# Kernel tuning notes

Hardware: AMD Instinct MI355X
Metric: run time of the kernel (lower is better)

Reference implementation:

```python
import jax, jax.numpy as jnp
import numpy as np

TOP_K = 2
TEMPERATURE = 1.0


def setup_inputs() -> dict:
    key = jax.random.key(0)
    k1, k2, k3 = jax.random.split(key, 3)
    x = jax.random.normal(k1, (4, 2048, 2048), jnp.float32)
    # prototypes are top right-singular vectors of lora_A -> unit norm rows
    protos = jax.random.normal(k2, (8, 2048), jnp.float32)
    protos = protos / jnp.linalg.norm(protos, axis=-1, keepdims=True)
    # precomputed_W = stack of B @ A per expert, shape (E, out, in)
    W = jax.random.normal(k3, (8, 2048, 2048), jnp.float32) * 0.02
    return {"x": x, "prototypes": protos, "W": W, "scaling": 2}


def reference(x, prototypes, W, scaling):
    F_in = x.shape[-1]
    tok = x.reshape(-1, F_in)                      # (t, F)
    t = tok.shape[0]
    E = prototypes.shape[0]
    # Arrow routing: |<tok, proto_e>| similarity, keep top-k, softmax
    sim = jnp.abs(tok @ prototypes.T)              # (t, E)
    top_v, idx = jax.lax.top_k(sim, TOP_K)         # (t, k)
    neg_inf = jnp.asarray(-jnp.inf, tok.dtype)
    full_score = jnp.full((t, E), neg_inf, dtype=tok.dtype)
    full_score = full_score.at[jnp.arange(t)[:, None], idx].set(top_v)
    coeff = jax.nn.softmax(full_score / TEMPERATURE, axis=1)  # (t, E), zero off top-k
    # dense per-expert LoRA delta, then coefficient combine (as in source)
    W_tok = jnp.einsum('eoi,ti->eto', W, tok)      # (E, t, out)
    delta = jnp.einsum('te,eto->to', coeff, W_tok) # (t, out)
    delta = jnp.asarray(scaling, delta.dtype) * delta  # dropout = identity (eval)
    return delta.reshape(*x.shape[:-1], delta.shape[-1])
```

## Files before the change

kernel.cpp:

```cpp
#include <hip/hip_runtime.h>

#define T_TOK 8192
#define F_IN  2048
#define F_OUT 2048
#define N_EXP 8
#define NKS   (F_IN / 64)
#define MAXTILES 144
#define RT_TPB 16
#define ROUTE_BLOCKS (T_TOK / RT_TPB)
#define CVT_BLOCKS   2048

typedef __attribute__((ext_vector_type(8))) short    short8;
typedef __attribute__((ext_vector_type(4))) float    f32x4;
typedef __attribute__((ext_vector_type(8))) _Float16 half8;
typedef unsigned short ushort;

#define AS1 __attribute__((address_space(1)))
#define AS3 __attribute__((address_space(3)))
#define GLOAD16(g, l) __builtin_amdgcn_global_load_lds((const AS1 unsigned int*)(g), \
                                                       (AS3 unsigned int*)(l), 16, 0, 0)

__device__ inline ushort f2bf(float f) {
    unsigned u = __float_as_uint(f);
    u += 0x7FFFu + ((u >> 16) & 1u);
    return (ushort)(u >> 16);
}

__device__ inline void top2_store(const float* s, int ti, float sc,
                                  int* sh_ei, float (*sh_cf)[2]) {
    float v0 = -1.f; int i0 = 0;
    #pragma unroll
    for (int e = 0; e < N_EXP; ++e) {
        const float a = fabsf(s[e]);
        if (a > v0) { v0 = a; i0 = e; }
    }
    float v1 = -1.f; int i1 = 0;
    #pragma unroll
    for (int e = 0; e < N_EXP; ++e) {
        const float a = fabsf(s[e]);
        if (e != i0 && a > v1) { v1 = a; i1 = e; }
    }
    const float ex  = expf(v1 - v0);
    const float inv = 1.f / (1.f + ex);
    sh_ei[ti]    = i0 | (i1 << 16);
    sh_cf[ti][0] = sc * inv;
    sh_cf[ti][1] = sc * ex * inv;
}

__global__ __launch_bounds__(256) void route_cvt_kernel(
    const float* __restrict__ x, const float* __restrict__ protos,
    const int* __restrict__ scaling, ushort* __restrict__ xb,
    int* __restrict__ counts, int* __restrict__ lists, float* __restrict__ coeffs,
    int* __restrict__ pos, const float* __restrict__ W, ushort* __restrict__ Wb)
{
    __shared__ int   sh_ei[RT_TPB];
    __shared__ float sh_cf[RT_TPB][2];
    __shared__ int   sh_base[N_EXP];

    if (blockIdx.x >= ROUTE_BLOCKS) {
        const int n8 = N_EXP * F_OUT * F_IN / 8;
        for (int i = (blockIdx.x - ROUTE_BLOCKS) * 256 + threadIdx.x; i < n8;
             i += CVT_BLOCKS * 256) {
            const float4 a = ((const float4*)W)[i * 2 + 0];
            const float4 b = ((const float4*)W)[i * 2 + 1];
            uint4 v;
            v.x = f2bf(a.x) | ((unsigned)f2bf(a.y) << 16);
            v.y = f2bf(a.z) | ((unsigned)f2bf(a.w) << 16);
            v.z = f2bf(b.x) | ((unsigned)f2bf(b.y) << 16);
            v.w = f2bf(b.z) | ((unsigned)f2bf(b.w) << 16);
            ((uint4*)Wb)[i] = v;
        }
        return;
    }

    const int wave = threadIdx.x >> 6;
    const int lane = threadIdx.x & 63;
    const float sc = (float)(*scaling);

    for (int pr = 0; pr < 2; ++pr) {
        const int ti0  = wave * 4 + pr * 2;
        const int tok0 = blockIdx.x * RT_TPB + ti0;
        const float* xr0 = x  + (size_t)tok0 * F_IN;
        const float* xr1 = xr0 + F_IN;
        ushort*      xo0 = xb + (size_t)tok0 * F_IN;
        ushort*      xo1 = xo0 + F_IN;

        float s0[N_EXP] = {}, s1[N_EXP] = {};
        for (int c = 0; c < F_IN / 256; ++c) {
            const int off = c * 256 + lane * 4;
            const float4 a = *(const float4*)(xr0 + off);
            const float4 b = *(const float4*)(xr1 + off);
            uint2 ba, bb;
            ba.x = f2bf(a.x) | ((unsigned)f2bf(a.y) << 16);
            ba.y = f2bf(a.z) | ((unsigned)f2bf(a.w) << 16);
            bb.x = f2bf(b.x) | ((unsigned)f2bf(b.y) << 16);
            bb.y = f2bf(b.z) | ((unsigned)f2bf(b.w) << 16);
            *(uint2*)(xo0 + off) = ba;
            *(uint2*)(xo1 + off) = bb;
            #pragma unroll
            for (int e = 0; e < N_EXP; ++e) {
                const float4 pv = *(const float4*)(protos + e * F_IN + off);
                s0[e] += a.x * pv.x + a.y * pv.y + a.z * pv.z + a.w * pv.w;
                s1[e] += b.x * pv.x + b.y * pv.y + b.z * pv.z + b.w * pv.w;
            }
        }
        #pragma unroll
        for (int e = 0; e < N_EXP; ++e) {
            float v0 = s0[e], v1 = s1[e];
            #pragma unroll
            for (int off = 32; off; off >>= 1) {
                v0 += __shfl_down(v0, off, 64);
                v1 += __shfl_down(v1, off, 64);
            }
            s0[e] = v0; s1[e] = v1;
        }
        if (lane == 0) {
            top2_store(s0, ti0,     sc, sh_ei, sh_cf);
            top2_store(s1, ti0 + 1, sc, sh_ei, sh_cf);
        }
    }
    __syncthreads();

    if (threadIdx.x < 64) {
        const int  p      = threadIdx.x;
        const bool active = p < RT_TPB * 2;
        const int  ti = p >> 1, j = p & 1;
        const int  e  = active ? ((sh_ei[ti] >> (j * 16)) & 0xffff) : 0xff;
        int rank = 0;
        #pragma unroll
        for (int ee = 0; ee < N_EXP; ++ee) {
            const unsigned long long m = __ballot(active && (e == ee));
            if (e == ee)
                rank = __popcll(m & ((1ull << p) - 1ull));
            if (p == ee && m != 0ull)
                sh_base[ee] = atomicAdd(&counts[ee], (int)__popcll(m));
        }
        if (active) {
            const int position = sh_base[e] + rank;
            const int gidx  = e * T_TOK + position;
            const int token = blockIdx.x * RT_TPB + ti;
            lists [gidx] = token;
            coeffs[gidx] = sh_cf[ti][j];
            pos[token * 2 + j] = gidx;
        }
    }
}

__global__ void plan_kernel(const int* __restrict__ counts, int* __restrict__ pbase,
                            int* __restrict__ ntiles, int* __restrict__ desc) {
    if (threadIdx.x == 0) {
        int pb = 0, t = 0;
        for (int e = 0; e < N_EXP; ++e) {
            pbase[e] = pb;
            const int ne = counts[e];
            const int nt = (ne + 127) >> 7;
            for (int i = 0; i < nt; ++i) desc[t++] = (e << 8) | i;
            pb += ne;
        }
        *ntiles = t;
    }
}

__global__ __launch_bounds__(256, 2) void gemm_kernel(
    const ushort* __restrict__ xb, const ushort* __restrict__ Wb,
    const int* __restrict__ counts, const int* __restrict__ lists,
    const int* __restrict__ pbase, const int* __restrict__ ntiles,
    const int* __restrict__ desc, _Float16* __restrict__ delta)
{
    const int total = *ntiles * 8;
    const int chunk = (total + 7) >> 3;
    const int xcd   = blockIdx.x & 7;
    const int j     = blockIdx.x >> 3;
    const int w     = xcd * chunk + j;
    if (j >= chunk || w >= total) return;
    const int ti = w >> 3;
    const int oi = w & 7;

    const int d     = desc[ti];
    const int e     = d >> 8;
    const int tile  = d & 255;
    const int n_e   = counts[e];
    const int tbase = tile << 7;
    const int o0    = oi * 256;
    const int prow0 = pbase[e] + tbase;

    __shared__ __align__(16) ushort As[128 * 64];
    __shared__ __align__(16) ushort Bs[256 * 64];

    const int tid  = threadIdx.x;
    const int lane = tid & 63;
    const int wid  = tid >> 6;
    const int wr   = wid >> 1, wc = wid & 1;

    const int ksrc = ((lane & 7) ^ (lane >> 3)) * 8;
    const ushort* srcA[4];
    #pragma unroll
    for (int g = 0; g < 4; ++g) {
        const int row  = g * 32 + wid * 8 + (lane >> 3);
        const int slot = min(tbase + row, n_e - 1);
        srcA[g] = xb + (size_t)lists[e * T_TOK + slot] * F_IN + ksrc;
    }
    const ushort* srcB = Wb + ((size_t)(e * F_OUT + o0 + wid * 8 + (lane >> 3))) * F_IN + ksrc;

    const int octx8 = ((lane >> 4) ^ (lane & 7)) * 8;
    const int ai    = (wr * 64  + (lane & 15)) * 64 + octx8;
    const int bi    = (wc * 128 + (lane & 15)) * 64 + octx8;

    f32x4 acc[4][8] = {};

    for (int ks = 0; ks < NKS; ++ks) {
        __syncthreads();
        #pragma unroll
        for (int g = 0; g < 4; ++g) {
            GLOAD16(srcA[g], As + (g * 32 + wid * 8) * 64);
            srcA[g] += 64;
        }
        #pragma unroll
        for (int g = 0; g < 8; ++g)
            GLOAD16(srcB + (size_t)g * 32 * F_IN, Bs + (g * 32 + wid * 8) * 64);
        srcB += 64;
        __syncthreads();

        short8 a[4][2], b[8][2];
        #pragma unroll
        for (int m = 0; m < 4; ++m) {
            a[m][0] = *(const short8*)(As + (ai + m * 1024));
            a[m][1] = *(const short8*)(As + ((ai + m * 1024) ^ 32));
        }
        #pragma unroll
        for (int n = 0; n < 8; ++n) {
            b[n][0] = *(const short8*)(Bs + (bi + n * 1024));
            b[n][1] = *(const short8*)(Bs + ((bi + n * 1024) ^ 32));
        }
        #pragma unroll
        for (int kk = 0; kk < 2; ++kk)
            #pragma unroll
            for (int m = 0; m < 4; ++m)
                #pragma unroll
                for (int n = 0; n < 8; ++n)
                    acc[m][n] = __builtin_amdgcn_mfma_f32_16x16x32_bf16(
                        a[m][kk], b[n][kk], acc[m][n], 0, 0, 0);
    }

    const int rl = (lane >> 4) * 4;
    const int cl = lane & 15;
    #pragma unroll
    for (int m = 0; m < 4; ++m)
        #pragma unroll
        for (int rr = 0; rr < 4; ++rr) {
            const int srow = wr * 64 + m * 16 + rl + rr;
            if (tbase + srow < n_e) {
                _Float16* drow = delta + (size_t)(prow0 + srow) * F_OUT + o0 + wc * 128 + cl;
                #pragma unroll
                for (int n = 0; n < 8; ++n)
                    drow[n * 16] = (_Float16)acc[m][n][rr];
            }
        }
}

__global__ __launch_bounds__(256) void combine_kernel(
    const _Float16* __restrict__ delta, const int* __restrict__ pos,
    const float* __restrict__ coeffs, const int* __restrict__ pbase,
    float* __restrict__ out)
{
    const int tok = blockIdx.x;
    const int id0 = pos[tok * 2 + 0];
    const int id1 = pos[tok * 2 + 1];
    const float cf0 = coeffs[id0];
    const float cf1 = coeffs[id1];
    const int r0 = pbase[id0 >> 13] + (id0 & (T_TOK - 1));
    const int r1 = pbase[id1 >> 13] + (id1 & (T_TOK - 1));
    const int c  = threadIdx.x * 8;

    const half8 a = *(const half8*)(delta + (size_t)r0 * F_OUT + c);
    const half8 b = *(const half8*)(delta + (size_t)r1 * F_OUT + c);
    float4 o0, o1;
    o0.x = cf0 * (float)a[0] + cf1 * (float)b[0];
    o0.y = cf0 * (float)a[1] + cf1 * (float)b[1];
    o0.z = cf0 * (float)a[2] + cf1 * (float)b[2];
    o0.w = cf0 * (float)a[3] + cf1 * (float)b[3];
    o1.x = cf0 * (float)a[4] + cf1 * (float)b[4];
    o1.y = cf0 * (float)a[5] + cf1 * (float)b[5];
    o1.z = cf0 * (float)a[6] + cf1 * (float)b[6];
    o1.w = cf0 * (float)a[7] + cf1 * (float)b[7];
    float* op = out + (size_t)tok * F_OUT + c;
    *(float4*)(op)     = o0;
    *(float4*)(op + 4) = o1;
}

extern "C" void kernel_launch(void* const* d_in, const int* in_sizes, int n_in,
                              void* d_out, int out_size, void* d_ws, size_t ws_size,
                              hipStream_t stream) {
    const float* x      = (const float*)d_in[0];
    const float* protos = (const float*)d_in[1];
    const float* W      = (const float*)d_in[2];
    const int*   scal   = (const int*)d_in[3];
    float* out = (float*)d_out;

    char* ws = (char*)d_ws;
    int*      counts = (int*)(ws + 0);
    int*      pbase  = (int*)(ws + 64);
    int*      ntiles = (int*)(ws + 128);
    int*      desc   = (int*)(ws + 256);
    int*      pos    = (int*)(ws + 65536);
    int*      lists  = (int*)(ws + 262144);
    float*    coeffs = (float*)(ws + 524288);
    ushort*   xb     = (ushort*)(ws + (1ull << 20));
    ushort*   Wb     = (ushort*)(ws + (36ull << 20));
    _Float16* delta  = (_Float16*)(ws + (104ull << 20));

    hipMemsetAsync(counts, 0, N_EXP * sizeof(int), stream);

    route_cvt_kernel<<<ROUTE_BLOCKS + CVT_BLOCKS, 256, 0, stream>>>(
        x, protos, scal, xb, counts, lists, coeffs, pos, W, Wb);
    plan_kernel<<<1, 64, 0, stream>>>(counts, pbase, ntiles, desc);

    gemm_kernel<<<MAXTILES * 8, 256, 0, stream>>>(xb, Wb, counts, lists, pbase, ntiles, desc, delta);

    combine_kernel<<<T_TOK, 256, 0, stream>>>(delta, pos, coeffs, pbase, out);
}
```

Before: 296.0 us.

## Fuse expert combine into GEMM epilogue via atomic adds into zeroed output

```diff
diff --git a/kernel.cpp b/kernel.cpp
--- a/kernel.cpp
+++ b/kernel.cpp
@@ -12,7 +12,6 @@
 
 typedef __attribute__((ext_vector_type(8))) short    short8;
 typedef __attribute__((ext_vector_type(4))) float    f32x4;
-typedef __attribute__((ext_vector_type(8))) _Float16 half8;
 typedef unsigned short ushort;
 
 #define AS1 __attribute__((address_space(1)))
@@ -51,7 +50,7 @@
     const float* __restrict__ x, const float* __restrict__ protos,
     const int* __restrict__ scaling, ushort* __restrict__ xb,
     int* __restrict__ counts, int* __restrict__ lists, float* __restrict__ coeffs,
-    int* __restrict__ pos, const float* __restrict__ W, ushort* __restrict__ Wb)
+    const float* __restrict__ W, ushort* __restrict__ Wb)
 {
     __shared__ int   sh_ei[RT_TPB];
     __shared__ float sh_cf[RT_TPB][2];
@@ -86,6 +85,7 @@
         ushort*      xo1 = xo0 + F_IN;
 
         float s0[N_EXP] = {}, s1[N_EXP] = {};
+        #pragma unroll
         for (int c = 0; c < F_IN / 256; ++c) {
             const int off = c * 256 + lane * 4;
             const float4 a = *(const float4*)(xr0 + off);
@@ -138,24 +138,19 @@
         if (active) {
             const int position = sh_base[e] + rank;
             const int gidx  = e * T_TOK + position;
-            const int token = blockIdx.x * RT_TPB + ti;
-            lists [gidx] = token;
+            lists [gidx] = blockIdx.x * RT_TPB + ti;
             coeffs[gidx] = sh_cf[ti][j];
-            pos[token * 2 + j] = gidx;
-        }
-    }
-}
-
-__global__ void plan_kernel(const int* __restrict__ counts, int* __restrict__ pbase,
+        }
+    }
+}
+
+__global__ void plan_kernel(const int* __restrict__ counts,
                             int* __restrict__ ntiles, int* __restrict__ desc) {
     if (threadIdx.x == 0) {
-        int pb = 0, t = 0;
+        int t = 0;
         for (int e = 0; e < N_EXP; ++e) {
-            pbase[e] = pb;
-            const int ne = counts[e];
-            const int nt = (ne + 127) >> 7;
+            const int nt = (counts[e] + 127) >> 7;
             for (int i = 0; i < nt; ++i) desc[t++] = (e << 8) | i;
-            pb += ne;
         }
         *ntiles = t;
     }
@@ -164,8 +159,8 @@
 __global__ __launch_bounds__(256, 2) void gemm_kernel(
     const ushort* __restrict__ xb, const ushort* __restrict__ Wb,
     const int* __restrict__ counts, const int* __restrict__ lists,
-    const int* __restrict__ pbase, const int* __restrict__ ntiles,
-    const int* __restrict__ desc, _Float16* __restrict__ delta)
+    const int* __restrict__ ntiles, const int* __restrict__ desc,
+    const float* __restrict__ coeffs, float* __restrict__ out)
 {
     const int total = *ntiles * 8;
     const int chunk = (total + 7) >> 3;
@@ -182,7 +177,6 @@
     const int n_e   = counts[e];
     const int tbase = tile << 7;
     const int o0    = oi * 256;
-    const int prow0 = pbase[e] + tbase;
 
     __shared__ __align__(16) ushort As[128 * 64];
     __shared__ __align__(16) ushort Bs[256 * 64];
@@ -250,42 +244,14 @@
         for (int rr = 0; rr < 4; ++rr) {
             const int srow = wr * 64 + m * 16 + rl + rr;
             if (tbase + srow < n_e) {
-                _Float16* drow = delta + (size_t)(prow0 + srow) * F_OUT + o0 + wc * 128 + cl;
+                const int   tok = lists [e * T_TOK + tbase + srow];
+                const float cf  = coeffs[e * T_TOK + tbase + srow];
+                float* orow = out + (size_t)tok * F_OUT + o0 + wc * 128 + cl;
                 #pragma unroll
                 for (int n = 0; n < 8; ++n)
-                    drow[n * 16] = (_Float16)acc[m][n][rr];
+                    atomicAdd(orow + n * 16, cf * acc[m][n][rr]);
             }
         }
-}
-
-__global__ __launch_bounds__(256) void combine_kernel(
-    const _Float16* __restrict__ delta, const int* __restrict__ pos,
-    const float* __restrict__ coeffs, const int* __restrict__ pbase,
-    float* __restrict__ out)
-{
-    const int tok = blockIdx.x;
-    const int id0 = pos[tok * 2 + 0];
-    const int id1 = pos[tok * 2 + 1];
-    const float cf0 = coeffs[id0];
-    const float cf1 = coeffs[id1];
-    const int r0 = pbase[id0 >> 13] + (id0 & (T_TOK - 1));
-    const int r1 = pbase[id1 >> 13] + (id1 & (T_TOK - 1));
-    const int c  = threadIdx.x * 8;
-
-    const half8 a = *(const half8*)(delta + (size_t)r0 * F_OUT + c);
-    const half8 b = *(const half8*)(delta + (size_t)r1 * F_OUT + c);
-    float4 o0, o1;
-    o0.x = cf0 * (float)a[0] + cf1 * (float)b[0];
-    o0.y = cf0 * (float)a[1] + cf1 * (float)b[1];
-    o0.z = cf0 * (float)a[2] + cf1 * (float)b[2];
-    o0.w = cf0 * (float)a[3] + cf1 * (float)b[3];
-    o1.x = cf0 * (float)a[4] + cf1 * (float)b[4];
-    o1.y = cf0 * (float)a[5] + cf1 * (float)b[5];
-    o1.z = cf0 * (float)a[6] + cf1 * (float)b[6];
-    o1.w = cf0 * (float)a[7] + cf1 * (float)b[7];
-    float* op = out + (size_t)tok * F_OUT + c;
-    *(float4*)(op)     = o0;
-    *(float4*)(op + 4) = o1;
 }
 
 extern "C" void kernel_launch(void* const* d_in, const int* in_sizes, int n_in,
@@ -298,24 +264,21 @@
     float* out = (float*)d_out;
 
     char* ws = (char*)d_ws;
-    int*      counts = (int*)(ws + 0);
-    int*      pbase  = (int*)(ws + 64);
-    int*      ntiles = (int*)(ws + 128);
-    int*      desc   = (int*)(ws + 256);
-    int*      pos    = (int*)(ws + 65536);
-    int*      lists  = (int*)(ws + 262144);
-    float*    coeffs = (float*)(ws + 524288);
-    ushort*   xb     = (ushort*)(ws + (1ull << 20));
-    ushort*   Wb     = (ushort*)(ws + (36ull << 20));
-    _Float16* delta  = (_Float16*)(ws + (104ull << 20));
+    int*    counts = (int*)(ws + 0);
+    int*    ntiles = (int*)(ws + 128);
+    int*    desc   = (int*)(ws + 256);
+    int*    lists  = (int*)(ws + 262144);
+    float*  coeffs = (float*)(ws + 524288);
+    ushort* xb     = (ushort*)(ws + (1ull << 20));
+    ushort* Wb     = (ushort*)(ws + (36ull << 20));
 
     hipMemsetAsync(counts, 0, N_EXP * sizeof(int), stream);
+    hipMemsetAsync(out, 0, (size_t)out_size * sizeof(float), stream);
 
     route_cvt_kernel<<<ROUTE_BLOCKS + CVT_BLOCKS, 256, 0, stream>>>(
-        x, protos, scal, xb, counts, lists, coeffs, pos, W, Wb);
-    plan_kernel<<<1, 64, 0, stream>>>(counts, pbase, ntiles, desc);
-
-    gemm_kernel<<<MAXTILES * 8, 256, 0, stream>>>(xb, Wb, counts, lists, pbase, ntiles, desc, delta);
-
-    combine_kernel<<<T_TOK, 256, 0, stream>>>(delta, pos, coeffs, pbase, out);
-}
+        x, protos, scal, xb, counts, lists, coeffs, W, Wb);
+    plan_kernel<<<1, 64, 0, stream>>>(counts, ntiles, desc);
+
+    gemm_kernel<<<MAXTILES * 8, 256, 0, stream>>>(
+        xb, Wb, counts, lists, ntiles, desc, coeffs, out);
+}
```

Result: slower. 423.7 us (+43.1%).
